# Performance work log

Hardware: AMD Instinct MI355X
Metric: run time of the kernel (lower is better)

The kernel has to match this reference:

```python
import jax, jax.numpy as jnp
import numpy as np

B, H0, C_IN, C_OUT, K = 8, 32, 512, 512, 3
H1 = 2 * H0  # 64, resolution after bilinear upsample


def _mod_conv(x, conv_w, s):
    """StyleGAN2 modulate+demodulate per-sample conv.
    x: [B,H,W,Cin]; conv_w: [k,k,Cin,Cout]; s: [B,Cout] style scales.
    Implemented as one grouped conv (groups=B) instead of a Python loop.
    """
    wp = conv_w[None] * s[:, None, None, None, :]              # [B,k,k,Cin,Cout]
    d = jax.lax.rsqrt(jnp.sum(wp * wp, axis=(1, 2, 3)) + 1e-8)  # [B,Cout] demod
    wp = wp * d[:, None, None, None, :]
    Bn, H, W, Ci = x.shape
    Co = wp.shape[-1]
    xg = jnp.transpose(x, (1, 2, 0, 3)).reshape(1, H, W, Bn * Ci)
    kg = jnp.transpose(wp, (1, 2, 3, 0, 4)).reshape(wp.shape[1], wp.shape[2], Ci, Bn * Co)
    out = jax.lax.conv_general_dilated(
        xg, kg, (1, 1), 'SAME',
        dimension_numbers=('NHWC', 'HWIO', 'NHWC'),
        feature_group_count=Bn)
    return jnp.transpose(out.reshape(H, W, Bn, Co), (2, 0, 1, 3))


def setup_inputs() -> dict:
    key = jax.random.key(0)
    ks = jax.random.split(key, 13)
    g = 0.02
    return {
        'x': jax.random.uniform(ks[0], (B, H0, H0, C_IN), jnp.float32),
        'w': jax.random.uniform(ks[1], (B, 512), jnp.float32),
        'noise': jax.random.uniform(ks[2], (1, 1, 1, C_OUT), jnp.float32),
        'y0_kernel': jax.random.normal(ks[3], (512, C_OUT), jnp.float32) * g,
        'y0_bias': jnp.zeros((C_OUT,), jnp.float32),
        'y1_kernel': jax.random.normal(ks[4], (512, C_OUT), jnp.float32) * g,
        'y1_bias': jnp.zeros((C_OUT,), jnp.float32),
        'conv0': jax.random.normal(ks[5], (K, K, C_IN, C_OUT), jnp.float32) * g,
        'conv1': jax.random.normal(ks[6], (K, K, C_OUT, C_OUT), jnp.float32) * g,
        'noise_scale0': jax.random.normal(ks[7], (B, H1, H1, C_OUT), jnp.float32) * g,
        'noise_scale1': jax.random.normal(ks[8], (B, H1, H1, C_OUT), jnp.float32) * g,
        'bias0': jax.random.normal(ks[9], (B, H1, H1, C_OUT), jnp.float32) * g,
        'bias1': jax.random.normal(ks[10], (B, H1, H1, C_OUT), jnp.float32) * g,
    }


def reference(x, w, noise, y0_kernel, y0_bias, y1_kernel, y1_bias,
              conv0, conv1, noise_scale0, noise_scale1, bias0, bias1):
    x = jax.image.resize(x, (x.shape[0], 2 * x.shape[1], 2 * x.shape[2], x.shape[3]),
                         method='bilinear')
    s0 = w @ y0_kernel + y0_bias                 # Dense y_0
    x = _mod_conv(x, conv0, s0)
    x = x + noise_scale0 * noise + bias0
    x = jax.nn.leaky_relu(x, 0.2)
    # NOTE: the original TF code computes the second modulated conv but never
    # assigns its result back to x (the tf.concat is missing). We replicate
    # that math faithfully: the conv output is computed and discarded.
    s1 = w @ y1_kernel + y1_bias
    _unused = _mod_conv(x, conv1, s1)
    x = x + noise_scale1 * noise + bias1
    return jax.nn.leaky_relu(x, 0.2)
```

## Files before the change

kernel.cpp:

```cpp
#include <hip/hip_runtime.h>
#include <stdint.h>

typedef __attribute__((ext_vector_type(8))) __bf16 bf16x8;
typedef __attribute__((ext_vector_type(4))) float f32x4;
typedef __attribute__((ext_vector_type(8))) unsigned short us8;

__device__ __forceinline__ unsigned short f2bf(float f) {
  unsigned u = __float_as_uint(f);
  unsigned r = u + 0x7fffu + ((u >> 16) & 1u);
  return (unsigned short)(r >> 16);
}

__device__ __forceinline__ void gload16(const void* gptr, void* lptr) {
  __builtin_amdgcn_global_load_lds(
      (const __attribute__((address_space(1))) void*)gptr,
      (__attribute__((address_space(3))) void*)lptr, 16, 0, 0);
}

__global__ void k_bpack(const float* __restrict__ conv0,
                        unsigned short* __restrict__ bpack,
                        float* __restrict__ wpart) {
  __shared__ float tile[64][65];
  int bx = blockIdx.x;
  int tap = bx >> 6, rem = bx & 63;
  int chunk = rem >> 3, cb = rem & 7;
  int ci0 = chunk << 6, co0 = cb << 6;
  int ty = threadIdx.x >> 6, tx = threadIdx.x & 63;
#pragma unroll
  for (int k = 0; k < 16; ++k) {
    int ci = (k << 2) + ty;
    tile[ci][tx] = conv0[((size_t)(tap * 512 + ci0 + ci)) * 512 + co0 + tx];
  }
  __syncthreads();
  float p = 0.f;
#pragma unroll
  for (int q = 0; q < 16; ++q) {
    float v = tile[(ty << 4) + q][tx];
    p += v * v;
  }
  __shared__ float red[4][64];
  red[ty][tx] = p;
  __syncthreads();
  if (ty == 0)
    wpart[(size_t)(chunk * 9 + tap) * 512 + co0 + tx] =
        red[0][tx] + red[1][tx] + red[2][tx] + red[3][tx];
#pragma unroll
  for (int s2 = 0; s2 < 2; ++s2) {
    int slot = (threadIdx.x << 1) + s2;
    int f = slot >> 6, l = slot & 63;
    int co16l = f >> 1, kk = f & 1;
    int col = (co16l << 4) + (l & 15);
    int cil = (kk << 5) + ((l >> 4) << 3);
    us8 o;
#pragma unroll
    for (int e = 0; e < 8; ++e) o[e] = f2bf(tile[cil + e][col]);
    size_t fi = (((size_t)chunk * 9 + tap) * 32 + (cb << 2) + co16l) * 2 + kk;
    *(us8*)(bpack + fi * 512 + (size_t)l * 8) = o;
  }
}

__global__ void k_scale(const float* __restrict__ w, const float* __restrict__ y0k,
                        const float* __restrict__ y0b, const float* __restrict__ wpart,
                        float* __restrict__ scale) {
  int g = blockIdx.x * 256 + threadIdx.x;
  int b = g >> 9, co = g & 511;
  float s = y0b[co];
  const float* wr = w + b * 512;
  for (int ci = 0; ci < 512; ++ci) s += wr[ci] * y0k[ci * 512 + co];
  float ws = 0.f;
  for (int r = 0; r < 72; ++r) ws += wpart[(size_t)r * 512 + co];
  scale[g] = s * rsqrtf(s * s * ws + 1e-8f);
}

__global__ void k_up(const float* __restrict__ x, unsigned short* __restrict__ xpad) {
  int gid = blockIdx.x * 256 + threadIdx.x;
  if (gid >= 8 * 66 * 66 * 64) return;
  int c0 = (gid & 63) << 3;
  int pos = gid >> 6;
  int xx = pos % 66;
  int t = pos / 66;
  int yy = t % 66;
  int b = t / 66;
  unsigned short* dst = xpad + (size_t)pos * 512 + c0;
  us8 o;
  if (yy == 0 || yy == 65 || xx == 0 || xx == 65) {
#pragma unroll
    for (int i = 0; i < 8; ++i) o[i] = 0;
  } else {
    int y = yy - 1, xq = xx - 1;
    int jy = y >> 1, jx = xq >> 1;
    int r0, r1, cx0, cx1;
    float ay0, ay1, ax0, ax1;
    if ((y & 1) == 0) { r0 = jy > 0 ? jy - 1 : 0; r1 = jy;
      ay0 = jy > 0 ? 0.25f : 0.f; ay1 = jy > 0 ? 0.75f : 1.f;
    } else { r0 = jy; r1 = jy < 31 ? jy + 1 : 31;
      ay0 = jy < 31 ? 0.75f : 1.f; ay1 = jy < 31 ? 0.25f : 0.f; }
    if ((xq & 1) == 0) { cx0 = jx > 0 ? jx - 1 : 0; cx1 = jx;
      ax0 = jx > 0 ? 0.25f : 0.f; ax1 = jx > 0 ? 0.75f : 1.f;
    } else { cx0 = jx; cx1 = jx < 31 ? jx + 1 : 31;
      ax0 = jx < 31 ? 0.75f : 1.f; ax1 = jx < 31 ? 0.25f : 0.f; }
    const float* base = x + (size_t)b * 32 * 32 * 512 + c0;
    const f32x4* q00 = (const f32x4*)(base + (size_t)(r0 * 32 + cx0) * 512);
    const f32x4* q01 = (const f32x4*)(base + (size_t)(r0 * 32 + cx1) * 512);
    const f32x4* q10 = (const f32x4*)(base + (size_t)(r1 * 32 + cx0) * 512);
    const f32x4* q11 = (const f32x4*)(base + (size_t)(r1 * 32 + cx1) * 512);
#pragma unroll
    for (int h = 0; h < 2; ++h) {
      f32x4 a = q00[h], bb = q01[h], c = q10[h], d = q11[h];
#pragma unroll
      for (int e = 0; e < 4; ++e) {
        float v = ay0 * (ax0 * a[e] + ax1 * bb[e]) + ay1 * (ax0 * c[e] + ax1 * d[e]);
        o[h * 4 + e] = f2bf(v);
      }
    }
  }
  *(us8*)dst = o;
}

__global__ __launch_bounds__(256) void k_conv(
    const unsigned short* __restrict__ xpad,
    const unsigned short* __restrict__ bpack,
    const float* __restrict__ scale,
    const float* __restrict__ noise,
    const float* __restrict__ ns0, const float* __restrict__ ns1,
    const float* __restrict__ bias0, const float* __restrict__ bias1,
    float* __restrict__ out)
{
  __shared__ __align__(16) unsigned short ldsA[2][16896];

  const int tid = threadIdx.x;
  const int wid = tid >> 6;
  const int lane = tid & 63;
  const int l15 = lane & 15, lhi = lane >> 4;

  const int bx = blockIdx.x;
  const int nblk = (bx >> 1) & 3;
  const int mblk = ((bx >> 3) << 1) | (bx & 1);
  const int b = mblk >> 5;
  const int y0 = (mblk & 31) << 1;
  const int co_base = (nblk << 7) + (wid << 5);

  f32x4 acc[8][2];
#pragma unroll
  for (int i = 0; i < 8; ++i) {
    acc[i][0] = f32x4{0.f, 0.f, 0.f, 0.f};
    acc[i][1] = f32x4{0.f, 0.f, 0.f, 0.f};
  }

  const size_t xb = (size_t)b * (66 * 66 * 512);
  const size_t wboff = (size_t)((nblk << 3) + (wid << 1)) * 1024 + (size_t)lane * 8;
  bf16x8 bq0[4], bq1[4];

  {
#pragma unroll
    for (int i = wid; i < 33; i += 4) {
      int g = (i << 6) + lane;
      int rx = g >> 3;
      int r = rx / 66;
      int xx = rx - r * 66;
      int cg = (g & 7) ^ (xx & 7);
      const unsigned short* src =
          xpad + xb + ((size_t)((y0 + r) * 66 + xx) << 9) + (cg << 3);
      gload16(src, (char*)ldsA[0] + (i << 10));
    }
    const unsigned short* wb = bpack + wboff;
#pragma unroll
    for (int ni = 0; ni < 2; ++ni)
#pragma unroll
      for (int kk = 0; kk < 2; ++kk)
        bq0[ni * 2 + kk] = *(const bf16x8*)(wb + ni * 1024 + kk * 512);
  }
  __syncthreads();

  for (int chunk = 0; chunk < 8; ++chunk) {
    const char* Acur = (const char*)ldsA[chunk & 1];
    const unsigned short* wb = bpack + (size_t)chunk * 294912 + wboff;

#pragma unroll
    for (int tap = 0; tap < 9; ++tap) {
      auto& cur = (tap & 1) ? bq1 : bq0;
      auto& nxt = (tap & 1) ? bq0 : bq1;
      if (tap < 8) {
#pragma unroll
        for (int ni = 0; ni < 2; ++ni)
#pragma unroll
          for (int kk = 0; kk < 2; ++kk)
            nxt[ni * 2 + kk] =
                *(const bf16x8*)(wb + (tap + 1) * 32768 + ni * 1024 + kk * 512);
      } else if (chunk < 7) {
#pragma unroll
        for (int ni = 0; ni < 2; ++ni)
#pragma unroll
          for (int kk = 0; kk < 2; ++kk)
            nxt[ni * 2 + kk] =
                *(const bf16x8*)(wb + 294912 + ni * 1024 + kk * 512);
      }
      if (tap == 0 && chunk < 7) {
        char* Anxt = (char*)ldsA[(chunk + 1) & 1];
        const int kc = (chunk + 1) << 6;
#pragma unroll
        for (int i = wid; i < 33; i += 4) {
          int g = (i << 6) + lane;
          int rx = g >> 3;
          int r = rx / 66;
          int xx = rx - r * 66;
          int cg = (g & 7) ^ (xx & 7);
          const unsigned short* src =
              xpad + xb + ((size_t)((y0 + r) * 66 + xx) << 9) + kc + (cg << 3);
          gload16(src, Anxt + (i << 10));
        }
      }
      const int ky = tap / 3, kx = tap - ky * 3;
      const int axor = ((l15 + kx) & 7) << 4;
#pragma unroll
      for (int kk = 0; kk < 2; ++kk) {
        const int kbyte = (((kk << 5) + (lhi << 3)) << 1);
        bf16x8 af[8];
#pragma unroll
        for (int mi = 0; mi < 8; ++mi) {
          int r = (mi >> 2) + ky;
          int xx = ((mi & 3) << 4) + l15 + kx;
          int off = ((r * 66 + xx) << 7) + (kbyte ^ axor);
          af[mi] = *(const bf16x8*)(Acur + off);
        }
        __builtin_amdgcn_s_setprio(1);
#pragma unroll
        for (int mi = 0; mi < 8; ++mi)
#pragma unroll
          for (int ni = 0; ni < 2; ++ni)
            acc[mi][ni] = __builtin_amdgcn_mfma_f32_16x16x32_bf16(
                af[mi], cur[ni * 2 + kk], acc[mi][ni], 0, 0, 0);
        __builtin_amdgcn_s_setprio(0);
      }
    }
#pragma unroll
    for (int i = 0; i < 4; ++i) bq0[i] = bq1[i];
    __syncthreads();
  }

  float* ldsE = (float*)ldsA + wid * 4224;
  float sc[2];
#pragma unroll
  for (int ni = 0; ni < 2; ++ni)
    sc[ni] = scale[(b << 9) + co_base + (ni << 4) + l15];
#pragma unroll
  for (int mi = 0; mi < 8; ++mi)
#pragma unroll
    for (int ni = 0; ni < 2; ++ni)
#pragma unroll
      for (int j = 0; j < 4; ++j) {
        int px = (mi << 4) + (lhi << 2) + j;
        ldsE[px * 33 + (ni << 4) + l15] = acc[mi][ni][j] * sc[ni];
      }
  const int qd = lane & 7;
  const int hh = lane >> 3;
  const f32x4 nz4 = *(const f32x4*)(noise + co_base + (qd << 2));
#pragma unroll
  for (int q = 0; q < 16; ++q) {
    int px = (q << 3) + hh;
    f32x4 v = *(const f32x4*)(ldsE + px * 33 + (qd << 2));
    int py = y0 + (px >> 6), xcol = px & 63;
    size_t idx = (((size_t)((b << 6) + py) << 6) + xcol) * 512 + co_base + (qd << 2);
    f32x4 a0 = *(const f32x4*)(ns0 + idx);
    f32x4 b0 = *(const f32x4*)(bias0 + idx);
    f32x4 a1 = *(const f32x4*)(ns1 + idx);
    f32x4 b1 = *(const f32x4*)(bias1 + idx);
    f32x4 o;
#pragma unroll
    for (int e = 0; e < 4; ++e) {
      float v0 = v[e] + a0[e] * nz4[e] + b0[e];
      v0 = fmaxf(v0, 0.2f * v0);
      v0 = v0 + a1[e] * nz4[e] + b1[e];
      o[e] = fmaxf(v0, 0.2f * v0);
    }
    *(f32x4*)(out + idx) = o;
  }
}

extern "C" void kernel_launch(void* const* d_in, const int* in_sizes, int n_in,
                              void* d_out, int out_size, void* d_ws, size_t ws_size,
                              hipStream_t stream) {
  const float* x     = (const float*)d_in[0];
  const float* w     = (const float*)d_in[1];
  const float* noise = (const float*)d_in[2];
  const float* y0k   = (const float*)d_in[3];
  const float* y0b   = (const float*)d_in[4];
  const float* conv0 = (const float*)d_in[7];
  const float* ns0   = (const float*)d_in[9];
  const float* ns1   = (const float*)d_in[10];
  const float* bias0 = (const float*)d_in[11];
  const float* bias1 = (const float*)d_in[12];
  float* out = (float*)d_out;

  char* ws = (char*)d_ws;
  unsigned short* xpad  = (unsigned short*)ws;
  unsigned short* bpack = (unsigned short*)(ws + 35684352);
  float* scale = (float*)(ws + 35684352 + 4718592);
  float* wpart = (float*)(ws + 35684352 + 4718592 + 16384);

  k_bpack<<<576, 256, 0, stream>>>(conv0, bpack, wpart);
  k_scale<<<16, 256, 0, stream>>>(w, y0k, y0b, wpart, scale);
  k_up<<<8712, 256, 0, stream>>>(x, xpad);
  k_conv<<<1024, 256, 0, stream>>>(xpad, bpack, scale, noise, ns0, ns1, bias0, bias1, out);
}
```

Measured before the change: 214.0 us.

## Reshape per-wave MFMA tile from 128x32 to 64x64 for better operand reuse

```diff
diff --git a/kernel.cpp b/kernel.cpp
--- a/kernel.cpp
+++ b/kernel.cpp
@@ -3,6 +3,7 @@
 
 typedef __attribute__((ext_vector_type(8))) __bf16 bf16x8;
 typedef __attribute__((ext_vector_type(4))) float f32x4;
+typedef __attribute__((ext_vector_type(2))) float f32x2;
 typedef __attribute__((ext_vector_type(8))) unsigned short us8;
 
 __device__ __forceinline__ unsigned short f2bf(float f) {
@@ -138,18 +139,18 @@
   const int mblk = ((bx >> 3) << 1) | (bx & 1);
   const int b = mblk >> 5;
   const int y0 = (mblk & 31) << 1;
-  const int co_base = (nblk << 7) + (wid << 5);
-
-  f32x4 acc[8][2];
-#pragma unroll
-  for (int i = 0; i < 8; ++i) {
-    acc[i][0] = f32x4{0.f, 0.f, 0.f, 0.f};
-    acc[i][1] = f32x4{0.f, 0.f, 0.f, 0.f};
-  }
+  const int wr = wid >> 1, wc = wid & 1;
+  const int co_base = (nblk << 7) + (wc << 6);
+
+  f32x4 acc[4][4];
+#pragma unroll
+  for (int i = 0; i < 4; ++i)
+#pragma unroll
+    for (int j = 0; j < 4; ++j) acc[i][j] = f32x4{0.f, 0.f, 0.f, 0.f};
 
   const size_t xb = (size_t)b * (66 * 66 * 512);
-  const size_t wboff = (size_t)((nblk << 3) + (wid << 1)) * 1024 + (size_t)lane * 8;
-  bf16x8 bq0[4], bq1[4];
+  const size_t wboff = (size_t)((nblk << 3) + (wc << 2)) * 1024 + (size_t)lane * 8;
+  bf16x8 bq0[8], bq1[8];
 
   {
 #pragma unroll
@@ -165,7 +166,7 @@
     }
     const unsigned short* wb = bpack + wboff;
 #pragma unroll
-    for (int ni = 0; ni < 2; ++ni)
+    for (int ni = 0; ni < 4; ++ni)
 #pragma unroll
       for (int kk = 0; kk < 2; ++kk)
         bq0[ni * 2 + kk] = *(const bf16x8*)(wb + ni * 1024 + kk * 512);
@@ -182,14 +183,14 @@
       auto& nxt = (tap & 1) ? bq0 : bq1;
       if (tap < 8) {
 #pragma unroll
-        for (int ni = 0; ni < 2; ++ni)
+        for (int ni = 0; ni < 4; ++ni)
 #pragma unroll
           for (int kk = 0; kk < 2; ++kk)
             nxt[ni * 2 + kk] =
                 *(const bf16x8*)(wb + (tap + 1) * 32768 + ni * 1024 + kk * 512);
       } else if (chunk < 7) {
 #pragma unroll
-        for (int ni = 0; ni < 2; ++ni)
+        for (int ni = 0; ni < 4; ++ni)
 #pragma unroll
           for (int kk = 0; kk < 2; ++kk)
             nxt[ni * 2 + kk] =
@@ -211,64 +212,65 @@
         }
       }
       const int ky = tap / 3, kx = tap - ky * 3;
+      const int r = wr + ky;
       const int axor = ((l15 + kx) & 7) << 4;
 #pragma unroll
       for (int kk = 0; kk < 2; ++kk) {
         const int kbyte = (((kk << 5) + (lhi << 3)) << 1);
-        bf16x8 af[8];
-#pragma unroll
-        for (int mi = 0; mi < 8; ++mi) {
-          int r = (mi >> 2) + ky;
-          int xx = ((mi & 3) << 4) + l15 + kx;
+        bf16x8 af[4];
+#pragma unroll
+        for (int mi = 0; mi < 4; ++mi) {
+          int xx = (mi << 4) + l15 + kx;
           int off = ((r * 66 + xx) << 7) + (kbyte ^ axor);
           af[mi] = *(const bf16x8*)(Acur + off);
         }
         __builtin_amdgcn_s_setprio(1);
 #pragma unroll
-        for (int mi = 0; mi < 8; ++mi)
-#pragma unroll
-          for (int ni = 0; ni < 2; ++ni)
+        for (int mi = 0; mi < 4; ++mi)
+#pragma unroll
+          for (int ni = 0; ni < 4; ++ni)
             acc[mi][ni] = __builtin_amdgcn_mfma_f32_16x16x32_bf16(
                 af[mi], cur[ni * 2 + kk], acc[mi][ni], 0, 0, 0);
         __builtin_amdgcn_s_setprio(0);
       }
     }
 #pragma unroll
-    for (int i = 0; i < 4; ++i) bq0[i] = bq1[i];
+    for (int i = 0; i < 8; ++i) bq0[i] = bq1[i];
     __syncthreads();
   }
 
   float* ldsE = (float*)ldsA + wid * 4224;
-  float sc[2];
-#pragma unroll
-  for (int ni = 0; ni < 2; ++ni)
+  float sc[4];
+#pragma unroll
+  for (int ni = 0; ni < 4; ++ni)
     sc[ni] = scale[(b << 9) + co_base + (ni << 4) + l15];
 #pragma unroll
-  for (int mi = 0; mi < 8; ++mi)
-#pragma unroll
-    for (int ni = 0; ni < 2; ++ni)
+  for (int mi = 0; mi < 4; ++mi)
+#pragma unroll
+    for (int ni = 0; ni < 4; ++ni)
 #pragma unroll
       for (int j = 0; j < 4; ++j) {
         int px = (mi << 4) + (lhi << 2) + j;
-        ldsE[px * 33 + (ni << 4) + l15] = acc[mi][ni][j] * sc[ni];
-      }
-  const int qd = lane & 7;
-  const int hh = lane >> 3;
+        ldsE[px * 66 + (ni << 4) + l15] = acc[mi][ni][j] * sc[ni];
+      }
+  const int qd = l15;
+  const int py = y0 + wr;
   const f32x4 nz4 = *(const f32x4*)(noise + co_base + (qd << 2));
 #pragma unroll
   for (int q = 0; q < 16; ++q) {
-    int px = (q << 3) + hh;
-    f32x4 v = *(const f32x4*)(ldsE + px * 33 + (qd << 2));
-    int py = y0 + (px >> 6), xcol = px & 63;
-    size_t idx = (((size_t)((b << 6) + py) << 6) + xcol) * 512 + co_base + (qd << 2);
+    int px = (q << 2) + lhi;
+    f32x2 v01 = *(const f32x2*)(ldsE + px * 66 + (qd << 2));
+    f32x2 v23 = *(const f32x2*)(ldsE + px * 66 + (qd << 2) + 2);
+    size_t idx = (((size_t)((b << 6) + py) << 6) + px) * 512 + co_base + (qd << 2);
     f32x4 a0 = *(const f32x4*)(ns0 + idx);
     f32x4 b0 = *(const f32x4*)(bias0 + idx);
     f32x4 a1 = *(const f32x4*)(ns1 + idx);
     f32x4 b1 = *(const f32x4*)(bias1 + idx);
     f32x4 o;
+    float vv[4] = {v01[0], v01[1], v23[0], v23[1]};
 #pragma unroll
     for (int e = 0; e < 4; ++e) {
-      float v0 = v[e] + a0[e] * nz4[e] + b0[e];
+      float v0 = vv[e] + a0[e] * nz4[e] + b0[e];
       v0 = fmaxf(v0, 0.2f * v0);
       v0 = v0 + a1[e] * nz4[e] + b1[e];
       o[e] = fmaxf(v0, 0.2f * v0);
```

New measurement: 215.4 us. No clear change (+0.6%).
